# Kernel tuning notes

Measured on AMD Instinct MI355X. Metric: run time of the kernel, lower is better.

Reference implementation:

```python
import jax, jax.numpy as jnp
import numpy as np

B, T, D = 512, 200, 64
VU, VI = 100000, 200000


def _init_params():
    ks = jax.random.split(jax.random.key(1), 12)
    g = lambda k, s, sc=0.05: jax.random.normal(k, s, dtype=jnp.float32) * sc
    return {
        "emb_user": g(ks[0], (VU, D)),
        "emb_item": g(ks[1], (VI, D)),
        "gru_Wx": g(ks[2], (D, 3 * D)),
        "gru_Wh": g(ks[3], (D, 3 * D)),
        "gru_b": jnp.zeros((3 * D,), jnp.float32),
        "aug_Wx": g(ks[4], (D, 3 * D)),
        "aug_Wh": g(ks[5], (D, 3 * D)),
        "aug_b": jnp.zeros((3 * D,), jnp.float32),
        "aux_W1": g(ks[6], (2 * D, 100)),
        "aux_b1": jnp.zeros((100,), jnp.float32),
        "aux_W2": g(ks[7], (100, 50)),
        "aux_b2": jnp.zeros((50,), jnp.float32),
        "aux_W3": g(ks[8], (50, 2)),
        "aux_b3": jnp.zeros((2,), jnp.float32),
        "bn_gamma": jnp.ones((2 * D,), jnp.float32),
        "bn_beta": jnp.zeros((2 * D,), jnp.float32),
        "fc_W1": g(ks[9], (2 * D, 200)),
        "fc_b1": jnp.zeros((200,), jnp.float32),
        "prelu_a1": jnp.zeros((200,), jnp.float32),
        "fc_W2": g(ks[10], (200, 80)),
        "fc_b2": jnp.zeros((80,), jnp.float32),
        "prelu_a2": jnp.zeros((80,), jnp.float32),
        "fc_W3": g(ks[11], (80, 2)),
        "fc_b3": jnp.zeros((2,), jnp.float32),
    }


def setup_inputs():
    key = jax.random.key(0)
    k1, k2, k3 = jax.random.split(key, 3)
    inp = {
        "user_ids": jax.random.randint(k1, (B,), 0, VU),
        "behavior_ids": jax.random.randint(k2, (B, T), 0, VI),
        "target_ids": jax.random.randint(k3, (B,), 0, VI),
    }
    inp.update(_init_params())
    return inp


def _gru(x, Wx, Wh, b):
    # x: [B,T,D]; precompute all input-side gate projections, scan over time
    xg = jnp.einsum("btd,de->bte", x, Wx) + b  # [B,T,3D]

    def step(h, xg_t):
        hg = h @ Wh[:, : 2 * D]
        z = jax.nn.sigmoid(xg_t[:, :D] + hg[:, :D])
        r = jax.nn.sigmoid(xg_t[:, D : 2 * D] + hg[:, D:])
        n = jnp.tanh(xg_t[:, 2 * D :] + (r * h) @ Wh[:, 2 * D :])
        h_new = z * h + (1.0 - z) * n
        return h_new, h_new

    h0 = jnp.zeros((x.shape[0], D), x.dtype)
    _, hs = jax.lax.scan(step, h0, jnp.swapaxes(xg, 0, 1))
    return jnp.swapaxes(hs, 0, 1)  # [B,T,D]


def _augru(x, att, Wx, Wh, b):
    # AUGRU: update gate scaled by attention score; returns final hidden [B,D]
    xg = jnp.einsum("btd,de->bte", x, Wx) + b

    def step(h, inputs):
        xg_t, a_t = inputs
        hg = h @ Wh[:, : 2 * D]
        u = jax.nn.sigmoid(xg_t[:, :D] + hg[:, :D])
        r = jax.nn.sigmoid(xg_t[:, D : 2 * D] + hg[:, D:])
        n = jnp.tanh(xg_t[:, 2 * D :] + (r * h) @ Wh[:, 2 * D :])
        u = a_t[:, None] * u
        h_new = (1.0 - u) * h + u * n
        return h_new, None

    h0 = jnp.zeros((x.shape[0], D), x.dtype)
    h, _ = jax.lax.scan(step, h0, (jnp.swapaxes(xg, 0, 1), att.T))
    return h


def _prelu(x, a):
    return jnp.maximum(x, 0.0) + a * jnp.minimum(x, 0.0)


def _forward(user_ids, behavior_ids, target_ids, p):
    user_emb = p["emb_user"][user_ids]          # [B,D]
    beh_emb = p["emb_item"][behavior_ids]       # [B,T,D]
    tgt_emb = p["emb_item"][target_ids]         # [B,D]

    gru_out = _gru(beh_emb, p["gru_Wx"], p["gru_Wh"], p["gru_b"])  # [B,T,D]

    # auxiliary loss: small MLP on (hidden, behavior emb) pairs, click class prob
    aux_in = jnp.concatenate([gru_out, beh_emb], axis=-1)  # [B,T,2D]
    h1 = jax.nn.relu(aux_in @ p["aux_W1"] + p["aux_b1"])
    h2 = jax.nn.relu(h1 @ p["aux_W2"] + p["aux_b2"])
    aux_logits = h2 @ p["aux_W3"] + p["aux_b3"]  # [B,T,2]
    aux_loss = -jnp.mean(jax.nn.log_softmax(aux_logits, axis=-1)[..., 0])

    # target-item attention over GRU hidden states (softmax over time)
    scores = jnp.einsum("bd,btd->bt", tgt_emb, gru_out)
    att = jax.nn.softmax(scores, axis=-1)  # [B,T]

    h_final = _augru(gru_out, att, p["aug_Wx"], p["aug_Wh"], p["aug_b"])  # [B,D]

    join = jnp.concatenate([h_final, user_emb], axis=-1)  # [B,2D]
    mu = jnp.mean(join, axis=0)
    var = jnp.var(join, axis=0)
    x = (join - mu) * jax.lax.rsqrt(var + 1e-3) * p["bn_gamma"] + p["bn_beta"]
    x = _prelu(jax.nn.relu(x @ p["fc_W1"] + p["fc_b1"]), p["prelu_a1"])
    x = _prelu(jax.nn.relu(x @ p["fc_W2"] + p["fc_b2"]), p["prelu_a2"])
    logit = x @ p["fc_W3"] + p["fc_b3"]  # [B,2]
    output = jax.nn.softmax(logit, axis=-1)
    return output, logit, aux_loss


def reference(user_ids, behavior_ids, target_ids, emb_user, emb_item, gru_Wx, gru_Wh, gru_b, aug_Wx, aug_Wh, aug_b, aux_W1, aux_b1, aux_W2, aux_b2, aux_W3, aux_b3, bn_gamma, bn_beta, fc_W1, fc_b1, prelu_a1, fc_W2, fc_b2, prelu_a2, fc_W3, fc_b3):
    p = dict(emb_user=emb_user, emb_item=emb_item, gru_Wx=gru_Wx, gru_Wh=gru_Wh, gru_b=gru_b,
             aug_Wx=aug_Wx, aug_Wh=aug_Wh, aug_b=aug_b, aux_W1=aux_W1, aux_b1=aux_b1,
             aux_W2=aux_W2, aux_b2=aux_b2, aux_W3=aux_W3, aux_b3=aux_b3,
             bn_gamma=bn_gamma, bn_beta=bn_beta, fc_W1=fc_W1, fc_b1=fc_b1, prelu_a1=prelu_a1,
             fc_W2=fc_W2, fc_b2=fc_b2, prelu_a2=prelu_a2, fc_W3=fc_W3, fc_b3=fc_b3)
    return _forward(user_ids, behavior_ids, target_ids, p)
```

## Files before the change

kernel.cpp:

```cpp
#include <hip/hip_runtime.h>
#include <hip/hip_bf16.h>
#include <math.h>

#define BB 512
#define TT 200
#define DD 64
#define G3 192
#define BT (BB*TT)

typedef __hip_bfloat16 bf16;
typedef short short8 __attribute__((ext_vector_type(8)));
typedef float f32x4 __attribute__((ext_vector_type(4)));

__device__ __forceinline__ float b2f(bf16 v){ return __bfloat162float(v); }
__device__ __forceinline__ float sigm(float x){ x = fminf(fmaxf(x,-30.f),30.f); return 1.f/(1.f+__expf(-x)); }
__device__ __forceinline__ float tanh_(float x){ x = fminf(fmaxf(x,-15.f),15.f); float e=__expf(2.f*x); return (e-1.f)/(e+1.f); }

__device__ __forceinline__ float ldv(const void* p, long i, int isbf){
  if (isbf) return __bfloat162float(((const bf16*)p)[i]);
  return ((const float*)p)[i];
}
__device__ __forceinline__ short f2bs(float f){
  union { bf16 b; short s; } u; u.b = __float2bfloat16(f); return u.s;
}
__device__ __forceinline__ float bs2f(short s){
  union { unsigned u; float f; } x; x.u = ((unsigned)(unsigned short)s) << 16; return x.f;
}
__device__ __forceinline__ unsigned pk2(int a, int b){
  return (((unsigned)a + 0x8000u) >> 16) | (((unsigned)b + 0x8000u) & 0xffff0000u);
}

__global__ void k_probe(const void* gamma, int* flag){
  if (threadIdx.x==0 && blockIdx.x==0)
    flag[0] = (((const unsigned*)gamma)[0] == 0x3F803F80u) ? 1 : 0;
}

__global__ __launch_bounds__(256) void k_prep(const void* W1, const void* W2, const void* b1,
    const void* b2, const void* W3, const void* b3, const void* gruWx, const void* augWx,
    short* w1t, short* w2t, float* b1f, float* b2f, float* w3f, float* b3f,
    short* wxg, short* wxa, const int* flagp){
  int isbf = *flagp;
  int gid = blockIdx.x*256 + threadIdx.x;
  int gstride = gridDim.x*256;
  for (int i = gid; i < 112*128; i += gstride){
    int n = i >> 7, k = i & 127;
    w1t[i] = f2bs((n < 100) ? ldv(W1, (long)k*100 + n, isbf) : 0.f);
  }
  for (int i = gid; i < 64*128; i += gstride){
    int n = i >> 7, k = i & 127;
    w2t[i] = f2bs((n < 50 && k < 100) ? ldv(W2, (long)k*50 + n, isbf) : 0.f);
  }
  for (int i = gid; i < 12288; i += gstride){
    int j = i & 7, L = (i >> 3) & 63, tk = i >> 9;
    int tile = tk >> 1, kb = tk & 1;
    int k = kb*32 + (L>>4)*8 + j, col = tile*16 + (L & 15);
    wxg[i] = f2bs(ldv(gruWx, (long)k*G3 + col, isbf));
    wxa[i] = f2bs(ldv(augWx, (long)k*G3 + col, isbf));
  }
  if (gid < 112) b1f[gid] = (gid < 100) ? ldv(b1, gid, isbf) : 0.f;
  if (gid < 64)  b2f[gid] = (gid < 50)  ? ldv(b2, gid, isbf) : 0.f;
  if (gid < 100) w3f[gid] = ldv(W3, gid, isbf);
  if (gid < 2)   b3f[gid] = ldv(b3, gid, isbf);
}

__global__ void k_gather(const int* __restrict__ uid, const int* __restrict__ tgt_id,
                         const void* __restrict__ eu, const void* __restrict__ ei,
                         float* __restrict__ tgt, float* __restrict__ usr, const int* flagp){
  int b = blockIdx.x, j = threadIdx.x;
  int isbf = *flagp;
  tgt[b*DD+j] = ldv(ei, (long)tgt_id[b]*DD + j, isbf);
  usr[b*DD+j] = ldv(eu, (long)uid[b]*DD + j, isbf);
}

template<bool GATHER>
__global__ __launch_bounds__(256) void k_xg(const short* __restrict__ wxf, const void* __restrict__ bias,
        const void* __restrict__ emb, const int* __restrict__ ids, const float* __restrict__ Ain,
        float* __restrict__ out, const int* flagp){
  __shared__ __align__(16) char lds[58112];
  int isbf = *flagp;
  int tid = threadIdx.x;
  long rbase = (long)blockIdx.x * 128;
  for (int i = tid; i < 1536; i += 256)
    *(short8*)(lds + i*16) = *(const short8*)(wxf + i*8);
  float* sB = (float*)(lds + 57344);
  if (tid < G3) sB[tid] = ldv(bias, tid, isbf);
  for (int u = tid; u < 1024; u += 256){
    int row = u >> 3, slot = u & 7;
    int off = row*128 + slot*16; off ^= (row&7)<<4;
    if (GATHER){
      long e = (long)ids[rbase+row]*DD + slot*8;
      short8 v;
      if (isbf) v = *(const short8*)((const short*)emb + e);
      else {
        const float* g = (const float*)emb + e;
        f32x4 f0 = *(const f32x4*)g;
        f32x4 f1 = *(const f32x4*)(g+4);
        v[0]=f2bs(f0[0]); v[1]=f2bs(f0[1]); v[2]=f2bs(f0[2]); v[3]=f2bs(f0[3]);
        v[4]=f2bs(f1[0]); v[5]=f2bs(f1[1]); v[6]=f2bs(f1[2]); v[7]=f2bs(f1[3]);
      }
      *(short8*)(lds + 24576 + off) = v;
    } else {
      const float* g = Ain + (rbase+row)*DD + slot*8;
      f32x4 f0 = *(const f32x4*)g;
      f32x4 f1 = *(const f32x4*)(g+4);
      short8 hi, lo;
      #pragma unroll
      for (int q=0;q<4;q++){
        hi[q] = f2bs(f0[q]); lo[q] = f2bs(f0[q] - bs2f(hi[q]));
        hi[4+q] = f2bs(f1[q]); lo[4+q] = f2bs(f1[q] - bs2f(hi[4+q]));
      }
      *(short8*)(lds + 24576 + off) = hi;
      *(short8*)(lds + 40960 + off) = lo;
    }
  }
  __syncthreads();
  int lane = tid & 63, w = tid >> 6;
  int m0 = w*32, lr = lane & 15, lg = lane >> 4;
  f32x4 acc[2][12];
  #pragma unroll
  for (int mi=0;mi<2;mi++){
    #pragma unroll
    for (int nt=0;nt<12;nt++){ acc[mi][nt][0]=0.f; acc[mi][nt][1]=0.f; acc[mi][nt][2]=0.f; acc[mi][nt][3]=0.f; }
  }
  #pragma unroll
  for (int ks=0; ks<2; ks++){
    short8 ah[2], al[2];
    #pragma unroll
    for (int mi=0; mi<2; mi++){
      int row = m0 + mi*16 + lr;
      int off = row*128 + ks*64 + lg*16; off ^= (row&7)<<4;
      ah[mi] = *(const short8*)(lds + 24576 + off);
      if (!GATHER) al[mi] = *(const short8*)(lds + 40960 + off);
    }
    #pragma unroll
    for (int nt=0; nt<12; nt++){
      short8 bf = *(const short8*)(lds + ((nt*2+ks)*64 + lane)*16);
      #pragma unroll
      for (int mi=0; mi<2; mi++){
        if (!GATHER) acc[mi][nt] = __builtin_amdgcn_mfma_f32_16x16x32_bf16(al[mi], bf, acc[mi][nt], 0,0,0);
        acc[mi][nt] = __builtin_amdgcn_mfma_f32_16x16x32_bf16(ah[mi], bf, acc[mi][nt], 0,0,0);
      }
    }
  }
  int r4 = lg*4;
  #pragma unroll
  for (int mi=0;mi<2;mi++){
    #pragma unroll
    for (int nt=0;nt<12;nt++){
      int n = nt*16 + lr;
      float bv = sB[n];
      #pragma unroll
      for (int i=0;i<4;i++){
        long row = rbase + m0 + mi*16 + r4 + i;
        out[row*G3 + n] = acc[mi][nt][i] + bv;
      }
    }
  }
}

template<bool AUG>
__global__ __launch_bounds__(64,1) void k_scan(const float* __restrict__ xg, const void* __restrict__ Whv,
    const float* __restrict__ att, float* __restrict__ hs_out, float* __restrict__ h_final,
    const int* flagp){
  int b = blockIdx.x, j = threadIdx.x;
  int isbf = *flagp;
  unsigned wz[32], wr[32], wn[32];
  if (isbf){
    const unsigned short* Wh = (const unsigned short*)Whv;
    #pragma unroll
    for (int q=0;q<32;q++){
      wz[q] = (unsigned)Wh[(2*q)*G3 + j]       | ((unsigned)Wh[(2*q+1)*G3 + j] << 16);
      wr[q] = (unsigned)Wh[(2*q)*G3 + 64 + j]  | ((unsigned)Wh[(2*q+1)*G3 + 64 + j] << 16);
      wn[q] = (unsigned)Wh[(2*q)*G3 + 128 + j] | ((unsigned)Wh[(2*q+1)*G3 + 128 + j] << 16);
    }
  } else {
    const float* Wh = (const float*)Whv;
    #pragma unroll
    for (int q=0;q<32;q++){
      wz[q] = (unsigned)(unsigned short)f2bs(Wh[(2*q)*G3 + j])
            | ((unsigned)(unsigned short)f2bs(Wh[(2*q+1)*G3 + j]) << 16);
      wr[q] = (unsigned)(unsigned short)f2bs(Wh[(2*q)*G3 + 64 + j])
            | ((unsigned)(unsigned short)f2bs(Wh[(2*q+1)*G3 + 64 + j]) << 16);
      wn[q] = (unsigned)(unsigned short)f2bs(Wh[(2*q)*G3 + 128 + j])
            | ((unsigned)(unsigned short)f2bs(Wh[(2*q+1)*G3 + 128 + j]) << 16);
    }
  }
  float hj = 0.f;
  const float* xgb = xg + (size_t)b*TT*G3 + j;
  const float* attb = att + (size_t)b*TT;
  float xz = xgb[0], xr = xgb[64], xn = xgb[128];
  float at = AUG ? attb[0] : 0.f;
  for (int t=0; t<TT; t++){
    int tp = (t+1 < TT) ? t+1 : t;
    const float* q_ = xgb + (size_t)tp*G3;
    float nxz = q_[0], nxr = q_[64], nxn = q_[128];
    float nat = AUG ? attb[tp] : 0.f;
    int hbits = __float_as_int(hj);
    int hsw = __builtin_amdgcn_ds_swizzle(hbits, 0x041F);
    int hpair = (int)pk2(hbits, hsw);
    unsigned hp[32];
    #pragma unroll
    for (int q=0;q<32;q++) hp[q] = (unsigned)__builtin_amdgcn_ds_bpermute(8*q, hpair);
    float az[4] = {xz, 0.f, 0.f, 0.f};
    float ar[4] = {xr, 0.f, 0.f, 0.f};
    #pragma unroll
    for (int q=0;q<32;q++){
      asm("v_dot2_f32_bf16 %0, %1, %2, %0" : "+v"(az[q&3]) : "v"(wz[q]), "v"(hp[q]));
      asm("v_dot2_f32_bf16 %0, %1, %2, %0" : "+v"(ar[q&3]) : "v"(wr[q]), "v"(hp[q]));
    }
    float z = sigm((az[0]+az[1])+(az[2]+az[3]));
    float r = sigm((ar[0]+ar[1])+(ar[2]+ar[3]));
    float u = AUG ? (at*z) : z;
    float rh = r*hj;
    int rbits = __float_as_int(rh);
    int rsw = __builtin_amdgcn_ds_swizzle(rbits, 0x041F);
    int rpair = (int)pk2(rbits, rsw);
    unsigned rp[32];
    #pragma unroll
    for (int q=0;q<32;q++) rp[q] = (unsigned)__builtin_amdgcn_ds_bpermute(8*q, rpair);
    float an[4] = {xn, 0.f, 0.f, 0.f};
    #pragma unroll
    for (int q=0;q<32;q++){
      asm("v_dot2_f32_bf16 %0, %1, %2, %0" : "+v"(an[q&3]) : "v"(wn[q]), "v"(rp[q]));
    }
    float n = tanh_((an[0]+an[1])+(an[2]+an[3]));
    float hnew = AUG ? ((1.f-u)*hj + u*n) : (u*hj + (1.f-u)*n);
    hj = hnew;
    if (!AUG) hs_out[((size_t)b*TT + t)*DD + j] = hnew;
    xz=nxz; xr=nxr; xn=nxn; at=nat;
  }
  if (AUG) h_final[b*DD + j] = hj;
}

__global__ __launch_bounds__(256) void k_att(const float* __restrict__ gru, const float* __restrict__ tgt,
                                             float* __restrict__ att){
  int b = blockIdx.x, tid = threadIdx.x;
  __shared__ float st[DD];
  __shared__ float red[256];
  if (tid < DD) st[tid] = tgt[b*DD + tid];
  __syncthreads();
  float s = 0.f;
  if (tid < TT){
    const float* g = gru + ((size_t)b*TT + tid)*DD;
    #pragma unroll
    for (int d=0; d<DD; d++) s += g[d]*st[d];
  }
  red[tid] = (tid<TT) ? s : -1e30f;
  __syncthreads();
  for (int w=128; w>0; w>>=1){ if (tid<w) red[tid] = fmaxf(red[tid], red[tid+w]); __syncthreads(); }
  float m = red[0];
  __syncthreads();
  float e = (tid<TT) ? __expf(s - m) : 0.f;
  red[tid] = e; __syncthreads();
  for (int w=128; w>0; w>>=1){ if (tid<w) red[tid] += red[tid+w]; __syncthreads(); }
  float inv = 1.f/red[0];
  if (tid < TT) att[b*TT + tid] = e*inv;
}

__global__ __launch_bounds__(256) void k_aux(const float* __restrict__ gru, const void* __restrict__ emb,
    const int* __restrict__ ids, const short* __restrict__ w1t, const short* __restrict__ w2t,
    const float* __restrict__ b1f, const float* __restrict__ b2f, const float* __restrict__ w3f,
    const float* __restrict__ b3f, float* __restrict__ part, const int* flagp){
  __shared__ __align__(16) char smem[78976];
  float* sb1 = (float*)(smem + 77824);
  float* sb2 = (float*)(smem + 78272);
  float* sw3 = (float*)(smem + 78528);
  float* sb3 = (float*)(smem + 78928);
  float* wred= (float*)(smem + 78936);
  int tid = threadIdx.x;
  int isbf = *flagp;
  long rbase = (long)blockIdx.x * 128;

  for (int i = tid; i < 1792; i += 256){
    int n = i >> 4, slot = i & 15;
    short8 v = *(const short8*)(w1t + n*128 + slot*8);
    int off = n*256 + slot*16; off ^= (n&7)<<4;
    *(short8*)(smem + 32768 + off) = v;
  }
  for (int i = tid; i < 1024; i += 256){
    int n = i >> 4, slot = i & 15;
    short8 v = *(const short8*)(w2t + n*128 + slot*8);
    int off = n*256 + slot*16; off ^= (n&7)<<4;
    *(short8*)(smem + 61440 + off) = v;
  }
  if (tid < 112) sb1[tid] = b1f[tid];
  if (tid < 100) sw3[tid] = w3f[tid];
  if (tid >= 112 && tid < 176) sb2[tid-112] = b2f[tid-112];
  if (tid >= 176 && tid < 178) sb3[tid-176] = b3f[tid-176];
  for (int i = tid; i < 2048; i += 256){
    int row = i >> 4, slot = i & 15, k0 = slot*8;
    short8 v;
    if (k0 < 64){
      const float* g = gru + (rbase+row)*64 + k0;
      f32x4 f0 = *(const f32x4*)g;
      f32x4 f1 = *(const f32x4*)(g+4);
      v[0]=f2bs(f0[0]); v[1]=f2bs(f0[1]); v[2]=f2bs(f0[2]); v[3]=f2bs(f0[3]);
      v[4]=f2bs(f1[0]); v[5]=f2bs(f1[1]); v[6]=f2bs(f1[2]); v[7]=f2bs(f1[3]);
    } else {
      long e = (long)ids[rbase+row]*64 + (k0-64);
      if (isbf){
        v = *(const short8*)((const short*)emb + e);
      } else {
        const float* g = (const float*)emb + e;
        f32x4 f0 = *(const f32x4*)g;
        f32x4 f1 = *(const f32x4*)(g+4);
        v[0]=f2bs(f0[0]); v[1]=f2bs(f0[1]); v[2]=f2bs(f0[2]); v[3]=f2bs(f0[3]);
        v[4]=f2bs(f1[0]); v[5]=f2bs(f1[1]); v[6]=f2bs(f1[2]); v[7]=f2bs(f1[3]);
      }
    }
    int off = row*256 + slot*16; off ^= (row&7)<<4;
    *(short8*)(smem + off) = v;
  }
  __syncthreads();

  int lane = tid & 63;
  int wv = tid >> 6;
  int m0 = wv * 32;
  int lrow = lane & 15;
  int kbL = ((lane >> 4) * 8) * 2;

  f32x4 acc1[2][7];
  #pragma unroll
  for (int mi=0;mi<2;mi++){
    #pragma unroll
    for (int ni=0;ni<7;ni++){ acc1[mi][ni][0]=0.f; acc1[mi][ni][1]=0.f; acc1[mi][ni][2]=0.f; acc1[mi][ni][3]=0.f; }
  }
  #pragma unroll
  for (int ks=0; ks<4; ks++){
    int kb = ks*64 + kbL;
    short8 af[2], bfv[7];
    #pragma unroll
    for (int mi=0; mi<2; mi++){
      int row = m0 + mi*16 + lrow;
      int off = row*256 + kb; off ^= (row&7)<<4;
      af[mi] = *(const short8*)(smem + off);
    }
    #pragma unroll
    for (int ni=0; ni<7; ni++){
      int n = ni*16 + lrow;
      int off = n*256 + kb; off ^= (n&7)<<4;
      bfv[ni] = *(const short8*)(smem + 32768 + off);
    }
    #pragma unroll
    for (int mi=0; mi<2; mi++){
      #pragma unroll
      for (int ni=0; ni<7; ni++)
        acc1[mi][ni] = __builtin_amdgcn_mfma_f32_16x16x32_bf16(af[mi], bfv[ni], acc1[mi][ni], 0, 0, 0);
    }
  }
  int lr4 = (lane >> 4) * 4;
  #pragma unroll
  for (int mi=0; mi<2; mi++){
    #pragma unroll
    for (int ni=0; ni<7; ni++){
      int col = ni*16 + lrow;
      float bias = sb1[col];
      #pragma unroll
      for (int i=0;i<4;i++){
        int row = m0 + mi*16 + lr4 + i;
        float v = fmaxf(acc1[mi][ni][i] + bias, 0.f);
        int off = row*256 + col*2; off ^= (row&7)<<4;
        *(short*)(smem + off) = f2bs(v);
      }
    }
  }
  {
    int row = m0 + (lane >> 1);
    int off = row*256 + (112 + (lane&1)*8)*2; off ^= (row&7)<<4;
    short8 z = {0,0,0,0,0,0,0,0};
    *(short8*)(smem + off) = z;
  }
  __syncthreads();

  f32x4 acc2[2][4];
  #pragma unroll
  for (int mi=0;mi<2;mi++){
    #pragma unroll
    for (int ni=0;ni<4;ni++){ acc2[mi][ni][0]=0.f; acc2[mi][ni][1]=0.f; acc2[mi][ni][2]=0.f; acc2[mi][ni][3]=0.f; }
  }
  #pragma unroll
  for (int ks=0; ks<4; ks++){
    int kb = ks*64 + kbL;
    short8 af[2], bgv[4];
    #pragma unroll
    for (int mi=0; mi<2; mi++){
      int row = m0 + mi*16 + lrow;
      int off = row*256 + kb; off ^= (row&7)<<4;
      af[mi] = *(const short8*)(smem + off);
    }
    #pragma unroll
    for (int ni=0; ni<4; ni++){
      int n = ni*16 + lrow;
      int off = n*256 + kb; off ^= (n&7)<<4;
      bgv[ni] = *(const short8*)(smem + 61440 + off);
    }
    #pragma unroll
    for (int mi=0; mi<2; mi++){
      #pragma unroll
      for (int ni=0; ni<4; ni++)
        acc2[mi][ni] = __builtin_amdgcn_mfma_f32_16x16x32_bf16(af[mi], bgv[ni], acc2[mi][ni], 0, 0, 0);
    }
  }
  #pragma unroll
  for (int mi=0; mi<2; mi++){
    #pragma unroll
    for (int ni=0; ni<4; ni++){
      int col = ni*16 + lrow;
      float bias = sb2[col];
      #pragma unroll
      for (int i=0;i<4;i++){
        int row = m0 + mi*16 + lr4 + i;
        float v = fmaxf(acc2[mi][ni][i] + bias, 0.f);
        *(short*)(smem + 32768 + row*136 + col*2) = f2bs(v);
      }
    }
  }
  __syncthreads();

  int row = tid >> 1, half = tid & 1;
  const short* h2r = (const short*)(smem + 32768) + row*68;
  float p0 = 0.f, p1 = 0.f;
  int kb0 = half*32, kb1 = half ? 50 : 32;
  for (int k=kb0; k<kb1; k++){
    float h = bs2f(h2r[k]);
    p0 += h*sw3[2*k]; p1 += h*sw3[2*k+1];
  }
  p0 += __shfl_xor(p0, 1, 64);
  p1 += __shfl_xor(p1, 1, 64);
  float l0 = p0 + sb3[0], l1 = p1 + sb3[1];
  float mx = fmaxf(l0, l1);
  float lse = mx + logf(__expf(l0-mx) + __expf(l1-mx));
  float c = (lse - l0) * 0.5f;
  #pragma unroll
  for (int off=32; off; off>>=1) c += __shfl_down(c, off, 64);
  if (lane == 0) wred[wv] = c;
  __syncthreads();
  if (tid == 0) part[blockIdx.x] = wred[0]+wred[1]+wred[2]+wred[3];
}

__global__ void k_auxred(const float* __restrict__ part, float* __restrict__ total){
  __shared__ float red[256];
  int tid = threadIdx.x;
  float s = 0.f;
  for (int i=tid; i<800; i+=256) s += part[i];
  red[tid]=s; __syncthreads();
  for (int w=128;w;w>>=1){ if(tid<w) red[tid]+=red[tid+w]; __syncthreads(); }
  if (tid==0) total[0]=red[0];
}

__global__ __launch_bounds__(64) void k_bn(const float* __restrict__ hf, const float* __restrict__ usr,
                                           float* __restrict__ bn){
  int c = blockIdx.x, l = threadIdx.x;
  const float* src = (c<64) ? (hf + c) : (usr + (c-64));
  float s=0.f, q=0.f;
  for (int r=l; r<BB; r+=64){ float v = src[(size_t)r*DD]; s+=v; q+=v*v; }
  #pragma unroll
  for (int off=32; off; off>>=1){ s += __shfl_down(s,off,64); q += __shfl_down(q,off,64); }
  if (l==0){
    float mean = s*(1.f/BB);
    float var = fmaxf(q*(1.f/BB) - mean*mean, 0.f);
    bn[c] = mean;
    bn[128+c] = rsqrtf(var + 1e-3f);
  }
}

template<typename WT>
__device__ __forceinline__ void fc_body(int b, int tid, const float* hf, const float* usr, const float* bn,
   const WT* gamma, const WT* beta, const WT* W1, const WT* b1, const WT* W2, const WT* b2,
   const WT* W3, const WT* b3, const float* auxsum, void* outv, int obf,
   float* xn, float* y1, float* y2){
  for (int c=tid; c<128; c+=64){
    float v = (c<64) ? hf[b*DD+c] : usr[b*DD + c-64];
    xn[c] = (v - bn[c])*bn[128+c]*b2f(gamma[c]) + b2f(beta[c]);
  }
  __syncthreads();
  #pragma unroll
  for (int i=0;i<4;i++){
    int n = tid + i*64;
    if (n < 200){
      float a = b2f(b1[n]);
      for (int k=0;k<128;k++) a += xn[k]*b2f(W1[k*200+n]);
      y1[n] = fmaxf(a, 0.f);
    }
  }
  __syncthreads();
  #pragma unroll
  for (int i=0;i<2;i++){
    int n = tid + i*64;
    if (n < 80){
      float a = b2f(b2[n]);
      for (int k=0;k<200;k++) a += y1[k]*b2f(W2[k*80+n]);
      y2[n] = fmaxf(a, 0.f);
    }
  }
  __syncthreads();
  float hv = y2[tid];
  float p0 = hv*b2f(W3[tid*2+0]);
  float p1 = hv*b2f(W3[tid*2+1]);
  if (tid < 16){
    float h2 = y2[tid+64];
    p0 += h2*b2f(W3[(tid+64)*2+0]);
    p1 += h2*b2f(W3[(tid+64)*2+1]);
  }
  #pragma unroll
  for (int off=32; off; off>>=1){ p0 += __shfl_down(p0,off,64); p1 += __shfl_down(p1,off,64); }
  if (tid==0){
    float l0 = p0 + b2f(b3[0]), l1 = p1 + b2f(b3[1]);
    float m = fmaxf(l0,l1);
    float e0 = __expf(l0-m), e1 = __expf(l1-m);
    float inv = 1.f/(e0+e1);
    float q0 = e0*inv, q1 = e1*inv;
    float al = auxsum[0] * (1.f/(float)BT);
    if (obf){
      bf16* o = (bf16*)outv;
      o[b*2+0] = __float2bfloat16(q0); o[b*2+1] = __float2bfloat16(q1);
      o[1024 + b*2+0] = __float2bfloat16(l0); o[1024 + b*2+1] = __float2bfloat16(l1);
      if (b==0) o[2048] = __float2bfloat16(al);
    } else {
      float* o = (float*)outv;
      o[b*2+0] = q0; o[b*2+1] = q1;
      o[1024 + b*2+0] = l0; o[1024 + b*2+1] = l1;
      if (b==0) o[2048] = al;
    }
  }
}

__global__ __launch_bounds__(64) void k_fc(const float* __restrict__ hf, const float* __restrict__ usr,
   const float* __restrict__ bn, const void* gamma, const void* beta,
   const void* W1, const void* b1, const void* W2, const void* b2,
   const void* W3, const void* b3, const float* __restrict__ auxsum,
   void* outv, const int* flagp){
  __shared__ float xn[128], y1[200], y2[80];
  int b = blockIdx.x, tid = threadIdx.x;
  int isbf = *flagp;
  if (isbf)
    fc_body<bf16>(b,tid,hf,usr,bn,(const bf16*)gamma,(const bf16*)beta,(const bf16*)W1,(const bf16*)b1,
                  (const bf16*)W2,(const bf16*)b2,(const bf16*)W3,(const bf16*)b3,auxsum,outv,1,xn,y1,y2);
  else
    fc_body<float>(b,tid,hf,usr,bn,(const float*)gamma,(const float*)beta,(const float*)W1,(const float*)b1,
                  (const float*)W2,(const float*)b2,(const float*)W3,(const float*)b3,auxsum,outv,0,xn,y1,y2);
}

extern "C" void kernel_launch(void* const* d_in, const int* in_sizes, int n_in,
                              void* d_out, int out_size, void* d_ws, size_t ws_size,
                              hipStream_t stream) {
  const int*  user_ids     = (const int*) d_in[0];
  const int*  behavior_ids = (const int*) d_in[1];
  const int*  target_ids   = (const int*) d_in[2];
  const void* emb_user = d_in[3];
  const void* emb_item = d_in[4];
  const void* gru_Wx   = d_in[5];
  const void* gru_Wh   = d_in[6];
  const void* gru_b    = d_in[7];
  const void* aug_Wx   = d_in[8];
  const void* aug_Wh   = d_in[9];
  const void* aug_b    = d_in[10];
  const void* aux_W1   = d_in[11];
  const void* aux_b1   = d_in[12];
  const void* aux_W2   = d_in[13];
  const void* aux_b2   = d_in[14];
  const void* aux_W3   = d_in[15];
  const void* aux_b3   = d_in[16];
  const void* bn_gamma = d_in[17];
  const void* bn_beta  = d_in[18];
  const void* fc_W1    = d_in[19];
  const void* fc_b1    = d_in[20];
  const void* fc_W2    = d_in[22];
  const void* fc_b2    = d_in[23];
  const void* fc_W3    = d_in[25];
  const void* fc_b3    = d_in[26];

  float* ws = (float*)d_ws;
  const size_t FLAG_OFF = 0;
  const size_t XG_OFF   = 16;
  const size_t GRU_OFF  = XG_OFF  + (size_t)BT*G3;
  const size_t ATT_OFF  = GRU_OFF + (size_t)BT*DD;
  const size_t TGT_OFF  = ATT_OFF + (size_t)BT;
  const size_t USR_OFF  = TGT_OFF + (size_t)BB*DD;
  const size_t HF_OFF   = USR_OFF + (size_t)BB*DD;
  const size_t BN_OFF   = HF_OFF  + (size_t)BB*DD;
  const size_t AUXP_OFF = BN_OFF  + 256;
  const size_t AUXS_OFF = AUXP_OFF + 800;
  const size_t W1T_OFF  = AUXS_OFF + 16;
  const size_t W2T_OFF  = W1T_OFF + 7168;
  const size_t B1F_OFF  = W2T_OFF + 4096;
  const size_t B2F_OFF  = B1F_OFF + 112;
  const size_t W3F_OFF  = B2F_OFF + 64;
  const size_t B3F_OFF  = W3F_OFF + 100;
  const size_t WXG_OFF  = B3F_OFF + 4;
  const size_t WXA_OFF  = WXG_OFF + 6144;
  const size_t END_OFF  = WXA_OFF + 6144;
  if (ws_size < END_OFF*sizeof(float)) return;

  int*   flag = (int*)(ws + FLAG_OFF);
  float* xg   = ws + XG_OFF;
  float* gruo = ws + GRU_OFF;
  float* att  = ws + ATT_OFF;
  float* tgt  = ws + TGT_OFF;
  float* usr  = ws + USR_OFF;
  float* hf   = ws + HF_OFF;
  float* bnst = ws + BN_OFF;
  float* auxp = ws + AUXP_OFF;
  float* auxs = ws + AUXS_OFF;
  short* w1t  = (short*)(ws + W1T_OFF);
  short* w2t  = (short*)(ws + W2T_OFF);
  float* b1f  = ws + B1F_OFF;
  float* b2f  = ws + B2F_OFF;
  float* w3f  = ws + W3F_OFF;
  float* b3f  = ws + B3F_OFF;
  short* wxg  = (short*)(ws + WXG_OFF);
  short* wxa  = (short*)(ws + WXA_OFF);

  k_probe<<<1, 64, 0, stream>>>(bn_gamma, flag);
  k_prep<<<8, 256, 0, stream>>>(aux_W1, aux_W2, aux_b1, aux_b2, aux_W3, aux_b3, gru_Wx, aug_Wx,
                                w1t, w2t, b1f, b2f, w3f, b3f, wxg, wxa, flag);
  k_gather<<<BB, 64, 0, stream>>>(user_ids, target_ids, emb_user, emb_item, tgt, usr, flag);
  k_xg<true><<<BT/128, 256, 0, stream>>>(wxg, gru_b, emb_item, behavior_ids, nullptr, xg, flag);
  k_scan<false><<<BB, 64, 0, stream>>>(xg, gru_Wh, nullptr, gruo, nullptr, flag);
  k_att<<<BB, 256, 0, stream>>>(gruo, tgt, att);
  k_aux<<<BT/128, 256, 0, stream>>>(gruo, emb_item, behavior_ids, w1t, w2t, b1f, b2f, w3f, b3f, auxp, flag);
  k_auxred<<<1, 256, 0, stream>>>(auxp, auxs);
  k_xg<false><<<BT/128, 256, 0, stream>>>(wxa, aug_b, nullptr, nullptr, gruo, xg, flag);
  k_scan<true><<<BB, 64, 0, stream>>>(xg, aug_Wh, att, nullptr, hf, flag);
  k_bn<<<128, 64, 0, stream>>>(hf, usr, bnst);
  k_fc<<<BB, 64, 0, stream>>>(hf, usr, bnst, bn_gamma, bn_beta, fc_W1, fc_b1, fc_W2, fc_b2, fc_W3, fc_b3, auxs, d_out, flag);
}
```

Baseline: 430.5 us.

## Merge independent stages into shared launches to overlap aux MLP with AUGRU scan

Independent kernels are combined into single launches that dispatch on block index: the embedding gather joins the first input projection, attention joins the second projection, and the aux-loss MLP blocks run alongside the AUGRU scan blocks, which now pack four batch rows per 256-thread block. The goal is to cut launch count and let the long, latency-bound scan overlap with the aux MLP work instead of running one after the other. The cost is larger shared-memory and register footprints per merged kernel, since each block reserves the union of both paths, which can lower occupancy. The launch_bounds(64,1) hint for the scan is also lost in the merged kernel.

```diff
diff --git a/kernel.cpp b/kernel.cpp
--- a/kernel.cpp
+++ b/kernel.cpp
@@ -63,23 +63,13 @@
   if (gid < 2)   b3f[gid] = ldv(b3, gid, isbf);
 }
 
-__global__ void k_gather(const int* __restrict__ uid, const int* __restrict__ tgt_id,
-                         const void* __restrict__ eu, const void* __restrict__ ei,
-                         float* __restrict__ tgt, float* __restrict__ usr, const int* flagp){
-  int b = blockIdx.x, j = threadIdx.x;
-  int isbf = *flagp;
-  tgt[b*DD+j] = ldv(ei, (long)tgt_id[b]*DD + j, isbf);
-  usr[b*DD+j] = ldv(eu, (long)uid[b]*DD + j, isbf);
-}
-
 template<bool GATHER>
-__global__ __launch_bounds__(256) void k_xg(const short* __restrict__ wxf, const void* __restrict__ bias,
+__device__ __forceinline__ void dev_xg(int bid, const short* __restrict__ wxf, const void* __restrict__ bias,
         const void* __restrict__ emb, const int* __restrict__ ids, const float* __restrict__ Ain,
-        float* __restrict__ out, const int* flagp){
+        float* __restrict__ out, int isbf){
   __shared__ __align__(16) char lds[58112];
-  int isbf = *flagp;
   int tid = threadIdx.x;
-  long rbase = (long)blockIdx.x * 128;
+  long rbase = (long)bid * 128;
   for (int i = tid; i < 1536; i += 256)
     *(short8*)(lds + i*16) = *(const short8*)(wxf + i*8);
   float* sB = (float*)(lds + 57344);
@@ -158,85 +148,11 @@
   }
 }
 
-template<bool AUG>
-__global__ __launch_bounds__(64,1) void k_scan(const float* __restrict__ xg, const void* __restrict__ Whv,
-    const float* __restrict__ att, float* __restrict__ hs_out, float* __restrict__ h_final,
-    const int* flagp){
-  int b = blockIdx.x, j = threadIdx.x;
-  int isbf = *flagp;
-  unsigned wz[32], wr[32], wn[32];
-  if (isbf){
-    const unsigned short* Wh = (const unsigned short*)Whv;
-    #pragma unroll
-    for (int q=0;q<32;q++){
-      wz[q] = (unsigned)Wh[(2*q)*G3 + j]       | ((unsigned)Wh[(2*q+1)*G3 + j] << 16);
-      wr[q] = (unsigned)Wh[(2*q)*G3 + 64 + j]  | ((unsigned)Wh[(2*q+1)*G3 + 64 + j] << 16);
-      wn[q] = (unsigned)Wh[(2*q)*G3 + 128 + j] | ((unsigned)Wh[(2*q+1)*G3 + 128 + j] << 16);
-    }
-  } else {
-    const float* Wh = (const float*)Whv;
-    #pragma unroll
-    for (int q=0;q<32;q++){
-      wz[q] = (unsigned)(unsigned short)f2bs(Wh[(2*q)*G3 + j])
-            | ((unsigned)(unsigned short)f2bs(Wh[(2*q+1)*G3 + j]) << 16);
-      wr[q] = (unsigned)(unsigned short)f2bs(Wh[(2*q)*G3 + 64 + j])
-            | ((unsigned)(unsigned short)f2bs(Wh[(2*q+1)*G3 + 64 + j]) << 16);
-      wn[q] = (unsigned)(unsigned short)f2bs(Wh[(2*q)*G3 + 128 + j])
-            | ((unsigned)(unsigned short)f2bs(Wh[(2*q+1)*G3 + 128 + j]) << 16);
-    }
-  }
-  float hj = 0.f;
-  const float* xgb = xg + (size_t)b*TT*G3 + j;
-  const float* attb = att + (size_t)b*TT;
-  float xz = xgb[0], xr = xgb[64], xn = xgb[128];
-  float at = AUG ? attb[0] : 0.f;
-  for (int t=0; t<TT; t++){
-    int tp = (t+1 < TT) ? t+1 : t;
-    const float* q_ = xgb + (size_t)tp*G3;
-    float nxz = q_[0], nxr = q_[64], nxn = q_[128];
-    float nat = AUG ? attb[tp] : 0.f;
-    int hbits = __float_as_int(hj);
-    int hsw = __builtin_amdgcn_ds_swizzle(hbits, 0x041F);
-    int hpair = (int)pk2(hbits, hsw);
-    unsigned hp[32];
-    #pragma unroll
-    for (int q=0;q<32;q++) hp[q] = (unsigned)__builtin_amdgcn_ds_bpermute(8*q, hpair);
-    float az[4] = {xz, 0.f, 0.f, 0.f};
-    float ar[4] = {xr, 0.f, 0.f, 0.f};
-    #pragma unroll
-    for (int q=0;q<32;q++){
-      asm("v_dot2_f32_bf16 %0, %1, %2, %0" : "+v"(az[q&3]) : "v"(wz[q]), "v"(hp[q]));
-      asm("v_dot2_f32_bf16 %0, %1, %2, %0" : "+v"(ar[q&3]) : "v"(wr[q]), "v"(hp[q]));
-    }
-    float z = sigm((az[0]+az[1])+(az[2]+az[3]));
-    float r = sigm((ar[0]+ar[1])+(ar[2]+ar[3]));
-    float u = AUG ? (at*z) : z;
-    float rh = r*hj;
-    int rbits = __float_as_int(rh);
-    int rsw = __builtin_amdgcn_ds_swizzle(rbits, 0x041F);
-    int rpair = (int)pk2(rbits, rsw);
-    unsigned rp[32];
-    #pragma unroll
-    for (int q=0;q<32;q++) rp[q] = (unsigned)__builtin_amdgcn_ds_bpermute(8*q, rpair);
-    float an[4] = {xn, 0.f, 0.f, 0.f};
-    #pragma unroll
-    for (int q=0;q<32;q++){
-      asm("v_dot2_f32_bf16 %0, %1, %2, %0" : "+v"(an[q&3]) : "v"(wn[q]), "v"(rp[q]));
-    }
-    float n = tanh_((an[0]+an[1])+(an[2]+an[3]));
-    float hnew = AUG ? ((1.f-u)*hj + u*n) : (u*hj + (1.f-u)*n);
-    hj = hnew;
-    if (!AUG) hs_out[((size_t)b*TT + t)*DD + j] = hnew;
-    xz=nxz; xr=nxr; xn=nxn; at=nat;
-  }
-  if (AUG) h_final[b*DD + j] = hj;
-}
-
-__global__ __launch_bounds__(256) void k_att(const float* __restrict__ gru, const float* __restrict__ tgt,
-                                             float* __restrict__ att){
-  int b = blockIdx.x, tid = threadIdx.x;
+__device__ __forceinline__ void dev_att(int b, const float* __restrict__ gru,
+                                        const float* __restrict__ tgt, float* __restrict__ att){
   __shared__ float st[DD];
   __shared__ float red[256];
+  int tid = threadIdx.x;
   if (tid < DD) st[tid] = tgt[b*DD + tid];
   __syncthreads();
   float s = 0.f;
@@ -257,10 +173,10 @@
   if (tid < TT) att[b*TT + tid] = e*inv;
 }
 
-__global__ __launch_bounds__(256) void k_aux(const float* __restrict__ gru, const void* __restrict__ emb,
+__device__ __forceinline__ void dev_aux(int abid, const float* __restrict__ gru, const void* __restrict__ emb,
     const int* __restrict__ ids, const short* __restrict__ w1t, const short* __restrict__ w2t,
     const float* __restrict__ b1f, const float* __restrict__ b2f, const float* __restrict__ w3f,
-    const float* __restrict__ b3f, float* __restrict__ part, const int* flagp){
+    const float* __restrict__ b3f, float* __restrict__ part, int isbf){
   __shared__ __align__(16) char smem[78976];
   float* sb1 = (float*)(smem + 77824);
   float* sb2 = (float*)(smem + 78272);
@@ -268,8 +184,7 @@
   float* sb3 = (float*)(smem + 78928);
   float* wred= (float*)(smem + 78936);
   int tid = threadIdx.x;
-  int isbf = *flagp;
-  long rbase = (long)blockIdx.x * 128;
+  long rbase = (long)abid * 128;
 
   for (int i = tid; i < 1792; i += 256){
     int n = i >> 4, slot = i & 15;
@@ -435,7 +350,184 @@
   for (int off=32; off; off>>=1) c += __shfl_down(c, off, 64);
   if (lane == 0) wred[wv] = c;
   __syncthreads();
-  if (tid == 0) part[blockIdx.x] = wred[0]+wred[1]+wred[2]+wred[3];
+  if (tid == 0) part[abid] = wred[0]+wred[1]+wred[2]+wred[3];
+}
+
+__device__ __forceinline__ void dev_scan_aug(int b, int j, const float* __restrict__ xg,
+    const void* __restrict__ Whv, const float* __restrict__ att, float* __restrict__ h_final, int isbf){
+  unsigned wz[32], wr[32], wn[32];
+  if (isbf){
+    const unsigned short* Wh = (const unsigned short*)Whv;
+    #pragma unroll
+    for (int q=0;q<32;q++){
+      wz[q] = (unsigned)Wh[(2*q)*G3 + j]       | ((unsigned)Wh[(2*q+1)*G3 + j] << 16);
+      wr[q] = (unsigned)Wh[(2*q)*G3 + 64 + j]  | ((unsigned)Wh[(2*q+1)*G3 + 64 + j] << 16);
+      wn[q] = (unsigned)Wh[(2*q)*G3 + 128 + j] | ((unsigned)Wh[(2*q+1)*G3 + 128 + j] << 16);
+    }
+  } else {
+    const float* Wh = (const float*)Whv;
+    #pragma unroll
+    for (int q=0;q<32;q++){
+      wz[q] = (unsigned)(unsigned short)f2bs(Wh[(2*q)*G3 + j])
+            | ((unsigned)(unsigned short)f2bs(Wh[(2*q+1)*G3 + j]) << 16);
+      wr[q] = (unsigned)(unsigned short)f2bs(Wh[(2*q)*G3 + 64 + j])
+            | ((unsigned)(unsigned short)f2bs(Wh[(2*q+1)*G3 + 64 + j]) << 16);
+      wn[q] = (unsigned)(unsigned short)f2bs(Wh[(2*q)*G3 + 128 + j])
+            | ((unsigned)(unsigned short)f2bs(Wh[(2*q+1)*G3 + 128 + j]) << 16);
+    }
+  }
+  float hj = 0.f;
+  const float* xgb = xg + (size_t)b*TT*G3 + j;
+  const float* attb = att + (size_t)b*TT;
+  float xz = xgb[0], xr = xgb[64], xn = xgb[128];
+  float at = attb[0];
+  for (int t=0; t<TT; t++){
+    int tp = (t+1 < TT) ? t+1 : t;
+    const float* q_ = xgb + (size_t)tp*G3;
+    float nxz = q_[0], nxr = q_[64], nxn = q_[128];
+    float nat = attb[tp];
+    int hbits = __float_as_int(hj);
+    int hsw = __builtin_amdgcn_ds_swizzle(hbits, 0x041F);
+    int hpair = (int)pk2(hbits, hsw);
+    unsigned hp[32];
+    #pragma unroll
+    for (int q=0;q<32;q++) hp[q] = (unsigned)__builtin_amdgcn_ds_bpermute(8*q, hpair);
+    float az[4] = {xz, 0.f, 0.f, 0.f};
+    float ar[4] = {xr, 0.f, 0.f, 0.f};
+    #pragma unroll
+    for (int q=0;q<32;q++){
+      asm("v_dot2_f32_bf16 %0, %1, %2, %0" : "+v"(az[q&3]) : "v"(wz[q]), "v"(hp[q]));
+      asm("v_dot2_f32_bf16 %0, %1, %2, %0" : "+v"(ar[q&3]) : "v"(wr[q]), "v"(hp[q]));
+    }
+    float z = sigm((az[0]+az[1])+(az[2]+az[3]));
+    float r = sigm((ar[0]+ar[1])+(ar[2]+ar[3]));
+    float u = at*z;
+    float rh = r*hj;
+    int rbits = __float_as_int(rh);
+    int rsw = __builtin_amdgcn_ds_swizzle(rbits, 0x041F);
+    int rpair = (int)pk2(rbits, rsw);
+    unsigned rp[32];
+    #pragma unroll
+    for (int q=0;q<32;q++) rp[q] = (unsigned)__builtin_amdgcn_ds_bpermute(8*q, rpair);
+    float an[4] = {xn, 0.f, 0.f, 0.f};
+    #pragma unroll
+    for (int q=0;q<32;q++){
+      asm("v_dot2_f32_bf16 %0, %1, %2, %0" : "+v"(an[q&3]) : "v"(wn[q]), "v"(rp[q]));
+    }
+    float n = tanh_((an[0]+an[1])+(an[2]+an[3]));
+    float hnew = (1.f-u)*hj + u*n;
+    hj = hnew;
+    xz=nxz; xr=nxr; xn=nxn; at=nat;
+  }
+  h_final[b*DD + j] = hj;
+}
+
+__global__ __launch_bounds__(64,1) void k_scan0(const float* __restrict__ xg, const void* __restrict__ Whv,
+    float* __restrict__ hs_out, const int* flagp){
+  int b = blockIdx.x, j = threadIdx.x;
+  int isbf = *flagp;
+  unsigned wz[32], wr[32], wn[32];
+  if (isbf){
+    const unsigned short* Wh = (const unsigned short*)Whv;
+    #pragma unroll
+    for (int q=0;q<32;q++){
+      wz[q] = (unsigned)Wh[(2*q)*G3 + j]       | ((unsigned)Wh[(2*q+1)*G3 + j] << 16);
+      wr[q] = (unsigned)Wh[(2*q)*G3 + 64 + j]  | ((unsigned)Wh[(2*q+1)*G3 + 64 + j] << 16);
+      wn[q] = (unsigned)Wh[(2*q)*G3 + 128 + j] | ((unsigned)Wh[(2*q+1)*G3 + 128 + j] << 16);
+    }
+  } else {
+    const float* Wh = (const float*)Whv;
+    #pragma unroll
+    for (int q=0;q<32;q++){
+      wz[q] = (unsigned)(unsigned short)f2bs(Wh[(2*q)*G3 + j])
+            | ((unsigned)(unsigned short)f2bs(Wh[(2*q+1)*G3 + j]) << 16);
+      wr[q] = (unsigned)(unsigned short)f2bs(Wh[(2*q)*G3 + 64 + j])
+            | ((unsigned)(unsigned short)f2bs(Wh[(2*q+1)*G3 + 64 + j]) << 16);
+      wn[q] = (unsigned)(unsigned short)f2bs(Wh[(2*q)*G3 + 128 + j])
+            | ((unsigned)(unsigned short)f2bs(Wh[(2*q+1)*G3 + 128 + j]) << 16);
+    }
+  }
+  float hj = 0.f;
+  const float* xgb = xg + (size_t)b*TT*G3 + j;
+  float xz = xgb[0], xr = xgb[64], xn = xgb[128];
+  for (int t=0; t<TT; t++){
+    int tp = (t+1 < TT) ? t+1 : t;
+    const float* q_ = xgb + (size_t)tp*G3;
+    float nxz = q_[0], nxr = q_[64], nxn = q_[128];
+    int hbits = __float_as_int(hj);
+    int hsw = __builtin_amdgcn_ds_swizzle(hbits, 0x041F);
+    int hpair = (int)pk2(hbits, hsw);
+    unsigned hp[32];
+    #pragma unroll
+    for (int q=0;q<32;q++) hp[q] = (unsigned)__builtin_amdgcn_ds_bpermute(8*q, hpair);
+    float az[4] = {xz, 0.f, 0.f, 0.f};
+    float ar[4] = {xr, 0.f, 0.f, 0.f};
+    #pragma unroll
+    for (int q=0;q<32;q++){
+      asm("v_dot2_f32_bf16 %0, %1, %2, %0" : "+v"(az[q&3]) : "v"(wz[q]), "v"(hp[q]));
+      asm("v_dot2_f32_bf16 %0, %1, %2, %0" : "+v"(ar[q&3]) : "v"(wr[q]), "v"(hp[q]));
+    }
+    float z = sigm((az[0]+az[1])+(az[2]+az[3]));
+    float r = sigm((ar[0]+ar[1])+(ar[2]+ar[3]));
+    float rh = r*hj;
+    int rbits = __float_as_int(rh);
+    int rsw = __builtin_amdgcn_ds_swizzle(rbits, 0x041F);
+    int rpair = (int)pk2(rbits, rsw);
+    unsigned rp[32];
+    #pragma unroll
+    for (int q=0;q<32;q++) rp[q] = (unsigned)__builtin_amdgcn_ds_bpermute(8*q, rpair);
+    float an[4] = {xn, 0.f, 0.f, 0.f};
+    #pragma unroll
+    for (int q=0;q<32;q++){
+      asm("v_dot2_f32_bf16 %0, %1, %2, %0" : "+v"(an[q&3]) : "v"(wn[q]), "v"(rp[q]));
+    }
+    float n = tanh_((an[0]+an[1])+(an[2]+an[3]));
+    float hnew = z*hj + (1.f-z)*n;
+    hj = hnew;
+    hs_out[((size_t)b*TT + t)*DD + j] = hnew;
+    xz=nxz; xr=nxr; xn=nxn;
+  }
+}
+
+__global__ __launch_bounds__(256) void k_xg1g(const short* __restrict__ wxf, const void* __restrict__ bias,
+    const void* __restrict__ embi, const int* __restrict__ beh_ids, float* __restrict__ out,
+    const int* __restrict__ uid, const int* __restrict__ tgt_id, const void* __restrict__ embu,
+    float* __restrict__ tgt, float* __restrict__ usr, const int* flagp){
+  int isbf = *flagp;
+  if (blockIdx.x < BT/128){
+    dev_xg<true>(blockIdx.x, wxf, bias, embi, beh_ids, nullptr, out, isbf);
+  } else {
+    int idx = blockIdx.x - BT/128;
+    int b = idx*4 + (threadIdx.x >> 6), j = threadIdx.x & 63;
+    tgt[b*DD+j] = ldv(embi, (long)tgt_id[b]*DD + j, isbf);
+    usr[b*DD+j] = ldv(embu, (long)uid[b]*DD + j, isbf);
+  }
+}
+
+__global__ __launch_bounds__(256) void k_xg2a(const short* __restrict__ wxf, const void* __restrict__ bias,
+    const float* __restrict__ gruo, float* __restrict__ out,
+    const float* __restrict__ tgt, float* __restrict__ att, const int* flagp){
+  int isbf = *flagp;
+  if (blockIdx.x < BT/128){
+    dev_xg<false>(blockIdx.x, wxf, bias, nullptr, nullptr, gruo, out, isbf);
+  } else {
+    dev_att(blockIdx.x - BT/128, gruo, tgt, att);
+  }
+}
+
+__global__ __launch_bounds__(256) void k_scan_aux(const float* __restrict__ xg, const void* __restrict__ Whv,
+    const float* __restrict__ att, float* __restrict__ h_final,
+    const float* __restrict__ gruo, const void* __restrict__ emb, const int* __restrict__ ids,
+    const short* __restrict__ w1t, const short* __restrict__ w2t,
+    const float* __restrict__ b1f, const float* __restrict__ b2f, const float* __restrict__ w3f,
+    const float* __restrict__ b3f, float* __restrict__ part, const int* flagp){
+  int isbf = *flagp;
+  if (blockIdx.x < 128){
+    int b = blockIdx.x*4 + (threadIdx.x >> 6);
+    dev_scan_aug(b, threadIdx.x & 63, xg, Whv, att, h_final, isbf);
+  } else {
+    dev_aux(blockIdx.x - 128, gruo, emb, ids, w1t, w2t, b1f, b2f, w3f, b3f, part, isbf);
+  }
 }
 
 __global__ void k_auxred(const float* __restrict__ part, float* __restrict__ total){
@@ -614,14 +706,14 @@
   k_probe<<<1, 64, 0, stream>>>(bn_gamma, flag);
   k_prep<<<8, 256, 0, stream>>>(aux_W1, aux_W2, aux_b1, aux_b2, aux_W3, aux_b3, gru_Wx, aug_Wx,
                                 w1t, w2t, b1f, b2f, w3f, b3f, wxg, wxa, flag);
-  k_gather<<<BB, 64, 0, stream>>>(user_ids, target_ids, emb_user, emb_item, tgt, usr, flag);
-  k_xg<true><<<BT/128, 256, 0, stream>>>(wxg, gru_b, emb_item, behavior_ids, nullptr, xg, flag);
-  k_scan<false><<<BB, 64, 0, stream>>>(xg, gru_Wh, nullptr, gruo, nullptr, flag);
-  k_att<<<BB, 256, 0, stream>>>(gruo, tgt, att);
-  k_aux<<<BT/128, 256, 0, stream>>>(gruo, emb_item, behavior_ids, w1t, w2t, b1f, b2f, w3f, b3f, auxp, flag);
+  k_xg1g<<<BT/128 + 128, 256, 0, stream>>>(wxg, gru_b, emb_item, behavior_ids, xg,
+                                           user_ids, target_ids, emb_user, tgt, usr, flag);
+  k_scan0<<<BB, 64, 0, stream>>>(xg, gru_Wh, gruo, flag);
+  k_xg2a<<<BT/128 + BB, 256, 0, stream>>>(wxa, aug_b, gruo, xg, tgt, att, flag);
+  k_scan_aux<<<128 + BT/128, 256, 0, stream>>>(xg, aug_Wh, att, hf,
+                                               gruo, emb_item, behavior_ids,
+                                               w1t, w2t, b1f, b2f, w3f, b3f, auxp, flag);
   k_auxred<<<1, 256, 0, stream>>>(auxp, auxs);
-  k_xg<false><<<BT/128, 256, 0, stream>>>(wxa, aug_b, nullptr, nullptr, gruo, xg, flag);
-  k_scan<true><<<BB, 64, 0, stream>>>(xg, aug_Wh, att, nullptr, hf, flag);
   k_bn<<<128, 64, 0, stream>>>(hf, usr, bnst);
   k_fc<<<BB, 64, 0, stream>>>(hf, usr, bnst, bn_gamma, bn_beta, fc_W1, fc_b1, fc_W2, fc_b2, fc_W3, fc_b3, auxs, d_out, flag);
 }
```

After: 394.8 us, median of 2. 8.3% less time.
